# Optimization experiments

Hardware: AMD Instinct MI355X
Metric: run time of the kernel (lower is better)

## Reference

```python
import jax, jax.numpy as jnp
import numpy as np

EMB_DIM = 300
VOCAB_X = 50000
VOCAB_Y = 50000
LEN_X = 64
LEN_Y = 64
BATCH = 1024
PAD_ID = 0


def setup_inputs() -> dict:
    key = jax.random.key(0)
    k1, k2, k3, k4, k5, k6, k7 = jax.random.split(key, 7)
    initrange = 0.5 / EMB_DIM
    emb_x = jax.random.uniform(k1, (VOCAB_X, EMB_DIM), jnp.float32, -initrange, initrange)
    emb_y = jax.random.uniform(k2, (VOCAB_Y, EMB_DIM), jnp.float32, -initrange, initrange)
    # padding row zeroed as in init_emb
    emb_x = emb_x.at[PAD_ID].set(0.0)
    emb_y = emb_y.at[PAD_ID].set(0.0)
    return {
        "samp_hid": jax.random.normal(k3, (BATCH, EMB_DIM), jnp.float32),
        "batch_x": jax.random.randint(k4, (BATCH, LEN_X), 0, VOCAB_X, jnp.int64 if jax.config.jax_enable_x64 else jnp.int32),
        "batch_y": jax.random.randint(k5, (BATCH, LEN_Y), 0, VOCAB_Y, jnp.int64 if jax.config.jax_enable_x64 else jnp.int32),
        "emb_x": emb_x,
        "emb_y": emb_y,
        "bias_x": jax.random.uniform(k6, (VOCAB_X,), jnp.float32),
        "bias_y": jax.random.uniform(k7, (VOCAB_Y,), jnp.float32),
    }


def _cal_nll(z, tokens, emb, bias):
    # logits shared across all positions: [B, V]
    logits = z @ emb.T + bias
    logp = jax.nn.log_softmax(logits, axis=-1)            # compute log-softmax ONCE per row
    tok_logp = jnp.take_along_axis(logp, tokens, axis=1)  # [B, L] gather per-position targets
    mask = (tokens != PAD_ID).astype(logits.dtype)        # CrossEntropyLoss(ignore_index=0)
    return jnp.sum(-tok_logp * mask, axis=1)              # sum over positions -> [B]


def reference(samp_hid, batch_x, batch_y, emb_x, emb_y, bias_x, bias_y):
    nll_x = _cal_nll(samp_hid, batch_x, emb_x, bias_x)
    nll_y = _cal_nll(samp_hid, batch_y, emb_y, bias_y)
    return jnp.mean(nll_x + nll_y)
```

## Files before the change

### kernel.cpp

```cpp
#include <hip/hip_runtime.h>

#define V_VOCAB 50000
#define K_DIM   300
#define NROWS   1024
#define LEN     64
#define NBC     392
#define NCG     1568
#define KS      19
#define PASSES  16
#define LOG2E   1.44269504088896f

typedef __attribute__((ext_vector_type(8)))  short bf16x8;
typedef __attribute__((ext_vector_type(16))) float f32x16;

static __device__ __forceinline__ unsigned short f2bf(float f) {
    unsigned int u = __builtin_bit_cast(unsigned int, f);
    u = u + 0x7fffu + ((u >> 16) & 1u);
    return (unsigned short)(u >> 16);
}

static __device__ __forceinline__ f32x16 zero16() {
    f32x16 z;
#pragma unroll
    for (int i = 0; i < 16; ++i) z[i] = 0.0f;
    return z;
}

static __device__ __forceinline__ float exp2_hw(float x) {
    float r;
    asm volatile("v_exp_f32 %0, %1" : "=v"(r) : "v"(x));
    return r;
}

static __device__ __forceinline__ void gload_lds16(const void* g, void* l) {
    __builtin_amdgcn_global_load_lds((const __attribute__((address_space(1))) void*)g,
                                     (__attribute__((address_space(3))) void*)l, 16, 0, 0);
}

__global__ void zbf_kernel(const float* __restrict__ z, unsigned short* __restrict__ zbf) {
    int t = blockIdx.x * 256 + threadIdx.x;
    int l    = t & 63;
    int rest = t >> 6;
    int ks   = rest % KS;
    int rblk = rest / KS;
    int row  = rblk * 32 + (l & 31);
    int k0   = ks * 16 + (l >> 5) * 8;
    unsigned short o[8];
#pragma unroll
    for (int j = 0; j < 8; ++j) {
        int k = k0 + j;
        float v = (k < K_DIM) ? z[row * K_DIM + k] * LOG2E
                              : ((k == K_DIM) ? LOG2E : 0.0f);
        o[j] = f2bf(v);
    }
    ushort4* p = (ushort4*)(zbf + (size_t)t * 8);
    p[0] = make_ushort4(o[0], o[1], o[2], o[3]);
    p[1] = make_ushort4(o[4], o[5], o[6], o[7]);
}

__global__ void __launch_bounds__(256, 2)
gemm_kernel(const unsigned short* __restrict__ zbf,
            const float* __restrict__ emb_x,
            const float* __restrict__ emb_y,
            const float* __restrict__ bias_x,
            const float* __restrict__ bias_y,
            float* __restrict__ partial,
            float* __restrict__ lsesum,
            int accmode) {
    __shared__ unsigned short Zs[2][19456];

    const int tid  = threadIdx.x;
    const int lane = tid & 63;
    const int w    = tid >> 6;
    const int side = blockIdx.y;
    const int bc   = blockIdx.x;
    const float* eg = side ? emb_y : emb_x;
    const float* bg = side ? bias_y : bias_x;

    {
        const unsigned short* src = zbf;
#pragma unroll
        for (int i = 0; i < 10; ++i) {
            int q = w * 10 + i;
            if (q >= 38) q -= 8;
            gload_lds16(src + (size_t)q * 512 + lane * 8, &Zs[0][q * 512]);
        }
    }

    bf16x8 a[KS];
    {
        const int c  = bc * 128 + w * 32 + (lane & 31);
        const bool cv = (c < V_VOCAB);
        const float* erow = eg + (size_t)c * K_DIM;
        const int khi = (lane >> 5) * 8;
#pragma unroll
        for (int ks = 0; ks < KS; ++ks) {
            const int k0 = ks * 16 + khi;
            float f[8];
            if (k0 + 8 <= K_DIM) {
                float4 u  = cv ? *(const float4*)(erow + k0)     : make_float4(0, 0, 0, 0);
                float4 v2 = cv ? *(const float4*)(erow + k0 + 4) : make_float4(0, 0, 0, 0);
                f[0] = u.x;  f[1] = u.y;  f[2] = u.z;  f[3] = u.w;
                f[4] = v2.x; f[5] = v2.y; f[6] = v2.z; f[7] = v2.w;
            } else {
#pragma unroll
                for (int j = 0; j < 8; ++j) {
                    int k = k0 + j;
                    f[j] = (k < K_DIM) ? (cv ? erow[k] : 0.0f)
                         : (k == K_DIM ? (cv ? bg[c] : -3e38f) : 0.0f);
                }
            }
            bf16x8 t;
#pragma unroll
            for (int j = 0; j < 8; ++j) t[j] = (short)f2bf(f[j]);
            a[ks] = t;
        }
    }

    float* pout = partial + ((size_t)side * NCG + (size_t)bc * 4 + w) * NROWS;
    float* lout = lsesum + side * NROWS;

    asm volatile("s_waitcnt vmcnt(0)" ::: "memory");
    __builtin_amdgcn_s_barrier();

    int buf = 0;
    for (int p = 0; p < PASSES; ++p) {
        if (p < PASSES - 1) {
            const unsigned short* src = zbf + (size_t)(p + 1) * 19456;
#pragma unroll
            for (int i = 0; i < 10; ++i) {
                int q = w * 10 + i;
                if (q >= 38) q -= 8;
                gload_lds16(src + (size_t)q * 512 + lane * 8, &Zs[buf ^ 1][q * 512]);
            }
        }

        const unsigned short* zb = &Zs[buf][0];
        f32x16 a0e = zero16(), a0o = zero16(), a1e = zero16(), a1o = zero16();
#pragma unroll
        for (int ks = 0; ks < KS; ks += 2) {
            bf16x8 b0 = *(const bf16x8*)(zb + ((size_t)ks * 64 + lane) * 8);
            a0e = __builtin_amdgcn_mfma_f32_32x32x16_bf16(a[ks], b0, a0e, 0, 0, 0);
            bf16x8 b1 = *(const bf16x8*)(zb + ((size_t)(KS + ks) * 64 + lane) * 8);
            a1e = __builtin_amdgcn_mfma_f32_32x32x16_bf16(a[ks], b1, a1e, 0, 0, 0);
            if (ks + 1 < KS) {
                bf16x8 c0 = *(const bf16x8*)(zb + ((size_t)(ks + 1) * 64 + lane) * 8);
                a0o = __builtin_amdgcn_mfma_f32_32x32x16_bf16(a[ks + 1], c0, a0o, 0, 0, 0);
                bf16x8 c1 = *(const bf16x8*)(zb + ((size_t)(KS + ks + 1) * 64 + lane) * 8);
                a1o = __builtin_amdgcn_mfma_f32_32x32x16_bf16(a[ks + 1], c1, a1o, 0, 0, 0);
            }
        }

        float s0 = 0.0f, s1 = 0.0f;
#pragma unroll
        for (int r = 0; r < 16; ++r) {
            s0 += exp2_hw(a0e[r] + a0o[r]);
            s1 += exp2_hw(a1e[r] + a1o[r]);
        }
        s0 += __shfl_xor(s0, 32, 64);
        s1 += __shfl_xor(s1, 32, 64);
        float val = (lane < 32) ? s0 : s1;
        if (accmode) { if (lane < 64) atomicAdd(lout + p * 64 + lane, val); }
        else         { pout[p * 64 + lane] = val; }

        asm volatile("s_waitcnt vmcnt(0)" ::: "memory");
        __builtin_amdgcn_s_barrier();
        buf ^= 1;
    }
}

__global__ void lse_kernel(const float* __restrict__ partial, float* __restrict__ lse) {
    __shared__ float red[1024];
    int side = blockIdx.x >> 4;
    int mg   = blockIdx.x & 15;
    int m    = mg * 64 + (threadIdx.x & 63);
    int sg   = threadIdx.x >> 6;
    const float* p = partial + (size_t)side * NCG * NROWS;
    float s = 0.0f;
    for (int cg = sg; cg < NCG; cg += 16)
        s += p[(size_t)cg * NROWS + m];
    red[threadIdx.x] = s;
    __syncthreads();
    if (threadIdx.x < 64) {
        float t = 0.0f;
#pragma unroll
        for (int j = 0; j < 16; ++j) t += red[threadIdx.x + 64 * j];
        lse[side * NROWS + mg * 64 + threadIdx.x] = logf(t);
    }
}

__global__ void lse_log_kernel(float* __restrict__ lsesum) {
    int g = blockIdx.x * 1024 + threadIdx.x;
    if (g < 2 * NROWS) lsesum[g] = logf(lsesum[g]);
}

__global__ void gatherdot_kernel(const float* __restrict__ z,
                                 const int* __restrict__ tok_x, const int* __restrict__ tok_y,
                                 const float* __restrict__ emb_x, const float* __restrict__ emb_y,
                                 const float* __restrict__ bias_x, const float* __restrict__ bias_y,
                                 const float* __restrict__ lse, float* __restrict__ gdpart) {
    __shared__ float gs[304];
    const int b = blockIdx.x, side = blockIdx.y & 1, half = blockIdx.y >> 1;
    const int tid = threadIdx.x;
    const int* tokp = (side ? tok_y : tok_x) + b * LEN + half * 32;
    const float* eg = side ? emb_y : emb_x;
    if (tid < K_DIM) {
        float g0 = 0.0f, g1 = 0.0f, g2 = 0.0f, g3 = 0.0f;
#pragma unroll 4
        for (int pos = 0; pos < 32; pos += 4) {
            int t0 = tokp[pos], t1 = tokp[pos + 1], t2 = tokp[pos + 2], t3 = tokp[pos + 3];
            if (t0) g0 += eg[(size_t)t0 * K_DIM + tid];
            if (t1) g1 += eg[(size_t)t1 * K_DIM + tid];
            if (t2) g2 += eg[(size_t)t2 * K_DIM + tid];
            if (t3) g3 += eg[(size_t)t3 * K_DIM + tid];
        }
        gs[tid] = (g0 + g1) + (g2 + g3);
    }
    __syncthreads();
    if (tid < 64) {
        const float* bg = side ? bias_y : bias_x;
        float dp = 0.0f;
#pragma unroll
        for (int i = 0; i < 5; ++i) {
            int d = tid + i * 64;
            if (d < K_DIM) dp += z[(size_t)b * K_DIM + d] * gs[d];
        }
        int t = (tid < 32) ? tokp[tid] : 0;
        float bs = t ? bg[t] : 0.0f;
        float ct = t ? 1.0f : 0.0f;
#pragma unroll
        for (int off = 32; off > 0; off >>= 1) {
            dp += __shfl_xor(dp, off, 64);
            bs += __shfl_xor(bs, off, 64);
            ct += __shfl_xor(ct, off, 64);
        }
        if (tid == 0)
            gdpart[((size_t)side * NROWS + b) * 2 + half] =
                ct * lse[side * NROWS + b] - dp - bs;
    }
}

__global__ void finalize_kernel(const float* __restrict__ gdpart, float* __restrict__ out) {
    __shared__ float r16[16];
    int i = threadIdx.x;
    float v = gdpart[i * 2] + gdpart[i * 2 + 1]
            + gdpart[(NROWS + i) * 2] + gdpart[(NROWS + i) * 2 + 1];
#pragma unroll
    for (int off = 32; off > 0; off >>= 1) v += __shfl_xor(v, off, 64);
    if ((i & 63) == 0) r16[i >> 6] = v;
    __syncthreads();
    if (i < 64) {
        float x = (i < 16) ? r16[i] : 0.0f;
#pragma unroll
        for (int off = 8; off > 0; off >>= 1) x += __shfl_xor(x, off, 64);
        if (i == 0) out[0] = x * (1.0f / 1024.0f);
    }
}

extern "C" void kernel_launch(void* const* d_in, const int* in_sizes, int n_in,
                              void* d_out, int out_size, void* d_ws, size_t ws_size,
                              hipStream_t stream) {
    const float* z      = (const float*)d_in[0];
    const int*   tok_x  = (const int*)d_in[1];
    const int*   tok_y  = (const int*)d_in[2];
    const float* emb_x  = (const float*)d_in[3];
    const float* emb_y  = (const float*)d_in[4];
    const float* bias_x = (const float*)d_in[5];
    const float* bias_y = (const float*)d_in[6];
    float* out = (float*)d_out;

    char* ws = (char*)d_ws;
    const size_t ZBF_B  = 622592;
    const size_t PART_B = (size_t)2 * NCG * NROWS * 4;
    const size_t need   = ZBF_B + PART_B + 8192 + 16384;

    unsigned short* zbf = (unsigned short*)ws;
    zbf_kernel<<<152, 256, 0, stream>>>(z, zbf);

    if (ws_size >= need) {
        float* partial = (float*)(ws + ZBF_B);
        float* lse     = (float*)(ws + ZBF_B + PART_B);
        float* gdpart  = (float*)(ws + ZBF_B + PART_B + 8192);
        gemm_kernel<<<dim3(NBC, 2), 256, 0, stream>>>(zbf, emb_x, emb_y, bias_x, bias_y,
                                                      partial, lse , 0);
        lse_kernel<<<32, 1024, 0, stream>>>(partial, lse);
        gatherdot_kernel<<<dim3(NROWS, 4), 320, 0, stream>>>(z, tok_x, tok_y, emb_x, emb_y,
                                                             bias_x, bias_y, lse, gdpart);
        finalize_kernel<<<1, 1024, 0, stream>>>(gdpart, out);
    } else {
        float* lse    = (float*)(ws + ZBF_B);
        float* gdpart = (float*)(ws + ZBF_B + 8192);
        hipMemsetAsync(lse, 0, 8192, stream);
        gemm_kernel<<<dim3(NBC, 2), 256, 0, stream>>>(zbf, emb_x, emb_y, bias_x, bias_y,
                                                      gdpart , lse, 1);
        lse_log_kernel<<<2, 1024, 0, stream>>>(lse);
        gatherdot_kernel<<<dim3(NROWS, 4), 320, 0, stream>>>(z, tok_x, tok_y, emb_x, emb_y,
                                                             bias_x, bias_y, lse, gdpart);
        finalize_kernel<<<1, 1024, 0, stream>>>(gdpart, out);
    }
}
```

Baseline: 169.1 us.

## Switch logits GEMM from bf16 to fp8 e4m3 MFMA with scaled embeddings

Converts z and the embedding tiles to fp8 e4m3 and uses the 32x32x16 fp8 MFMA instead of bf16. This halves the LDS slab size and the bytes moved for z. The embedding is prescaled by 512 to stay in fp8 range, and the bias moves out of the K padding into a per-fragment fp32 add folded into the exp2 argument. It also drops the 2-block occupancy hint from launch bounds. The cost is much lower precision in the logits, which risks log-sum-exp accuracy against the tolerance, plus per-element fp8 conversion cost.

```diff
diff --git a/kernel.cpp b/kernel.cpp
--- a/kernel.cpp
+++ b/kernel.cpp
@@ -1,4 +1,5 @@
 #include <hip/hip_runtime.h>
+#include <hip/hip_fp8.h>
 
 #define V_VOCAB 50000
 #define K_DIM   300
@@ -9,14 +10,14 @@
 #define KS      19
 #define PASSES  16
 #define LOG2E   1.44269504088896f
-
-typedef __attribute__((ext_vector_type(8)))  short bf16x8;
+#define INV512  0.001953125f
+#define SLAB_B  19456
+
 typedef __attribute__((ext_vector_type(16))) float f32x16;
 
-static __device__ __forceinline__ unsigned short f2bf(float f) {
-    unsigned int u = __builtin_bit_cast(unsigned int, f);
-    u = u + 0x7fffu + ((u >> 16) & 1u);
-    return (unsigned short)(u >> 16);
+static __device__ __forceinline__ unsigned char f2e4m3(float f) {
+    __hip_fp8_e4m3 h(f);
+    return (unsigned char)h.__x;
 }
 
 static __device__ __forceinline__ f32x16 zero16() {
@@ -37,29 +38,27 @@
                                      (__attribute__((address_space(3))) void*)l, 16, 0, 0);
 }
 
-__global__ void zbf_kernel(const float* __restrict__ z, unsigned short* __restrict__ zbf) {
+__global__ void zbf_kernel(const float* __restrict__ z, unsigned char* __restrict__ zbf) {
     int t = blockIdx.x * 256 + threadIdx.x;
+    if (t >= 32 * KS * 64) return;
     int l    = t & 63;
     int rest = t >> 6;
     int ks   = rest % KS;
     int rblk = rest / KS;
     int row  = rblk * 32 + (l & 31);
     int k0   = ks * 16 + (l >> 5) * 8;
-    unsigned short o[8];
+    union { unsigned char b[8]; unsigned long long u; } o;
 #pragma unroll
     for (int j = 0; j < 8; ++j) {
         int k = k0 + j;
-        float v = (k < K_DIM) ? z[row * K_DIM + k] * LOG2E
-                              : ((k == K_DIM) ? LOG2E : 0.0f);
-        o[j] = f2bf(v);
-    }
-    ushort4* p = (ushort4*)(zbf + (size_t)t * 8);
-    p[0] = make_ushort4(o[0], o[1], o[2], o[3]);
-    p[1] = make_ushort4(o[4], o[5], o[6], o[7]);
-}
-
-__global__ void __launch_bounds__(256, 2)
-gemm_kernel(const unsigned short* __restrict__ zbf,
+        float v = (k < K_DIM) ? z[row * K_DIM + k] * LOG2E : 0.0f;
+        o.b[j] = f2e4m3(v);
+    }
+    *(unsigned long long*)(zbf + (size_t)t * 8) = o.u;
+}
+
+__global__ void __launch_bounds__(256)
+gemm_kernel(const unsigned char* __restrict__ zbf,
             const float* __restrict__ emb_x,
             const float* __restrict__ emb_y,
             const float* __restrict__ bias_x,
@@ -67,7 +66,7 @@
             float* __restrict__ partial,
             float* __restrict__ lsesum,
             int accmode) {
-    __shared__ unsigned short Zs[2][19456];
+    __shared__ unsigned char Zs[2][SLAB_B];
 
     const int tid  = threadIdx.x;
     const int lane = tid & 63;
@@ -78,16 +77,16 @@
     const float* bg = side ? bias_y : bias_x;
 
     {
-        const unsigned short* src = zbf;
-#pragma unroll
-        for (int i = 0; i < 10; ++i) {
-            int q = w * 10 + i;
-            if (q >= 38) q -= 8;
-            gload_lds16(src + (size_t)q * 512 + lane * 8, &Zs[0][q * 512]);
-        }
-    }
-
-    bf16x8 a[KS];
+        const unsigned char* src = zbf;
+#pragma unroll
+        for (int i = 0; i < 5; ++i) {
+            int q = w * 5 + i;
+            if (q > 18) q = 18;
+            gload_lds16(src + (size_t)q * 1024 + lane * 16, &Zs[0][q * 1024]);
+        }
+    }
+
+    long a[KS];
     {
         const int c  = bc * 128 + w * 32 + (lane & 31);
         const bool cv = (c < V_VOCAB);
@@ -97,23 +96,26 @@
         for (int ks = 0; ks < KS; ++ks) {
             const int k0 = ks * 16 + khi;
             float f[8];
-            if (k0 + 8 <= K_DIM) {
-                float4 u  = cv ? *(const float4*)(erow + k0)     : make_float4(0, 0, 0, 0);
-                float4 v2 = cv ? *(const float4*)(erow + k0 + 4) : make_float4(0, 0, 0, 0);
-                f[0] = u.x;  f[1] = u.y;  f[2] = u.z;  f[3] = u.w;
-                f[4] = v2.x; f[5] = v2.y; f[6] = v2.z; f[7] = v2.w;
-            } else {
-#pragma unroll
-                for (int j = 0; j < 8; ++j) {
-                    int k = k0 + j;
-                    f[j] = (k < K_DIM) ? (cv ? erow[k] : 0.0f)
-                         : (k == K_DIM ? (cv ? bg[c] : -3e38f) : 0.0f);
-                }
+#pragma unroll
+            for (int j = 0; j < 8; ++j) {
+                int k = k0 + j;
+                f[j] = (cv && k < K_DIM) ? erow[k] * 512.0f : 0.0f;
             }
-            bf16x8 t;
-#pragma unroll
-            for (int j = 0; j < 8; ++j) t[j] = (short)f2bf(f[j]);
-            a[ks] = t;
+            union { unsigned char b[8]; long l; } u;
+#pragma unroll
+            for (int j = 0; j < 8; ++j) u.b[j] = f2e4m3(f[j]);
+            a[ks] = u.l;
+        }
+    }
+
+    float bias_frag[16];
+    {
+        const int h = lane >> 5;
+        const int cbase = bc * 128 + w * 32;
+#pragma unroll
+        for (int r = 0; r < 16; ++r) {
+            int c = cbase + (r & 3) + 8 * (r >> 2) + 4 * h;
+            bias_frag[r] = (c < V_VOCAB) ? LOG2E * bg[c] : -1e30f;
         }
     }
 
@@ -126,41 +128,41 @@
     int buf = 0;
     for (int p = 0; p < PASSES; ++p) {
         if (p < PASSES - 1) {
-            const unsigned short* src = zbf + (size_t)(p + 1) * 19456;
-#pragma unroll
-            for (int i = 0; i < 10; ++i) {
-                int q = w * 10 + i;
-                if (q >= 38) q -= 8;
-                gload_lds16(src + (size_t)q * 512 + lane * 8, &Zs[buf ^ 1][q * 512]);
+            const unsigned char* src = zbf + (size_t)(p + 1) * SLAB_B;
+#pragma unroll
+            for (int i = 0; i < 5; ++i) {
+                int q = w * 5 + i;
+                if (q > 18) q = 18;
+                gload_lds16(src + (size_t)q * 1024 + lane * 16, &Zs[buf ^ 1][q * 1024]);
             }
         }
 
-        const unsigned short* zb = &Zs[buf][0];
+        const unsigned char* zb = &Zs[buf][0];
         f32x16 a0e = zero16(), a0o = zero16(), a1e = zero16(), a1o = zero16();
 #pragma unroll
         for (int ks = 0; ks < KS; ks += 2) {
-            bf16x8 b0 = *(const bf16x8*)(zb + ((size_t)ks * 64 + lane) * 8);
-            a0e = __builtin_amdgcn_mfma_f32_32x32x16_bf16(a[ks], b0, a0e, 0, 0, 0);
-            bf16x8 b1 = *(const bf16x8*)(zb + ((size_t)(KS + ks) * 64 + lane) * 8);
-            a1e = __builtin_amdgcn_mfma_f32_32x32x16_bf16(a[ks], b1, a1e, 0, 0, 0);
+            long b0 = *(const long*)(zb + ((size_t)ks * 64 + lane) * 8);
+            a0e = __builtin_amdgcn_mfma_f32_32x32x16_fp8_fp8(a[ks], b0, a0e, 0, 0, 0);
+            long b1 = *(const long*)(zb + ((size_t)(KS + ks) * 64 + lane) * 8);
+            a1e = __builtin_amdgcn_mfma_f32_32x32x16_fp8_fp8(a[ks], b1, a1e, 0, 0, 0);
             if (ks + 1 < KS) {
-                bf16x8 c0 = *(const bf16x8*)(zb + ((size_t)(ks + 1) * 64 + lane) * 8);
-                a0o = __builtin_amdgcn_mfma_f32_32x32x16_bf16(a[ks + 1], c0, a0o, 0, 0, 0);
-                bf16x8 c1 = *(const bf16x8*)(zb + ((size_t)(KS + ks + 1) * 64 + lane) * 8);
-                a1o = __builtin_amdgcn_mfma_f32_32x32x16_bf16(a[ks + 1], c1, a1o, 0, 0, 0);
+                long c0 = *(const long*)(zb + ((size_t)(ks + 1) * 64 + lane) * 8);
+                a0o = __builtin_amdgcn_mfma_f32_32x32x16_fp8_fp8(a[ks + 1], c0, a0o, 0, 0, 0);
+                long c1 = *(const long*)(zb + ((size_t)(KS + ks + 1) * 64 + lane) * 8);
+                a1o = __builtin_amdgcn_mfma_f32_32x32x16_fp8_fp8(a[ks + 1], c1, a1o, 0, 0, 0);
             }
         }
 
         float s0 = 0.0f, s1 = 0.0f;
 #pragma unroll
         for (int r = 0; r < 16; ++r) {
-            s0 += exp2_hw(a0e[r] + a0o[r]);
-            s1 += exp2_hw(a1e[r] + a1o[r]);
+            s0 += exp2_hw(fmaf(a0e[r] + a0o[r], INV512, bias_frag[r]));
+            s1 += exp2_hw(fmaf(a1e[r] + a1o[r], INV512, bias_frag[r]));
         }
         s0 += __shfl_xor(s0, 32, 64);
         s1 += __shfl_xor(s1, 32, 64);
         float val = (lane < 32) ? s0 : s1;
-        if (accmode) { if (lane < 64) atomicAdd(lout + p * 64 + lane, val); }
+        if (accmode) { atomicAdd(lout + p * 64 + lane, val); }
         else         { pout[p * 64 + lane] = val; }
 
         asm volatile("s_waitcnt vmcnt(0)" ::: "memory");
@@ -270,11 +272,11 @@
     float* out = (float*)d_out;
 
     char* ws = (char*)d_ws;
-    const size_t ZBF_B  = 622592;
+    const size_t ZBF_B  = 311296;
     const size_t PART_B = (size_t)2 * NCG * NROWS * 4;
     const size_t need   = ZBF_B + PART_B + 8192 + 16384;
 
-    unsigned short* zbf = (unsigned short*)ws;
+    unsigned char* zbf = (unsigned char*)ws;
     zbf_kernel<<<152, 256, 0, stream>>>(z, zbf);
 
     if (ws_size >= need) {
```

After: 240.5 us. 1.42x slower.
